# Optimization experiments

Hardware: AMD Instinct MI355X
Metric: run time of the kernel (lower is better)

## Reference

```python
import jax, jax.numpy as jnp
import numpy as np

NORMALIZED_LENGTH = 512  # init kwarg
T_FRAMES = 32768
N_LM = 543  # mediapipe holistic landmark count


def setup_inputs() -> dict:
    key = jax.random.key(0)
    kf, kn, kd, ki = jax.random.split(key, 4)
    frames = jax.random.uniform(kf, (T_FRAMES, N_LM, 3), dtype=jnp.float32)
    nan_mask = jax.random.uniform(kn, (T_FRAMES, N_LM, 3)) < 0.10
    frames = jnp.where(nan_mask, jnp.float32(jnp.nan), frames)
    drop = jax.random.uniform(kd, (T_FRAMES,)) < 0.05
    hand_zone = jnp.arange(N_LM) >= 468
    frames = jnp.where(drop[:, None, None] & hand_zone[None, :, None], jnp.float32(jnp.nan), frames)
    lips_idx = jax.random.randint(ki, (40,), 0, 468, dtype=jnp.int32)
    return {"frames": frames, "lips_idx": lips_idx}


def _nan_mean0(x):
    # tf_nan_mean over axis 0 (keepdims); 0/0 -> NaN in TF is immediately zeroed
    # afterwards, so we emit 0 directly (identical forward values, safe grads).
    finite = ~jnp.isnan(x)
    s = jnp.where(finite, x, jnp.zeros((), x.dtype)).sum(axis=0, keepdims=True)
    c = finite.sum(axis=0, keepdims=True)
    return jnp.where(c == 0, jnp.zeros((), x.dtype), s / jnp.maximum(c, 1).astype(x.dtype))


def reference(frames, lips_idx):
    fr = frames[:, :, :2]                       # drop z coord
    lh = fr[:, 468:489]                         # [T, 21, 2]
    rh = fr[:, 522:543]                         # [T, 21, 2]
    lh = jnp.stack([lh[..., 0], 1.0 - lh[..., 1]], axis=-1)
    rh = jnp.stack([1.0 - rh[..., 0], 1.0 - rh[..., 1]], axis=-1)
    # stack hands, NaN->0, sum over the 2-hand axis
    hand = jnp.nan_to_num(lh) + jnp.nan_to_num(rh)   # [T, 21, 2]
    keep = hand.sum(axis=(1, 2)) != 0.0              # frames with >=1 visible hand
    hand = hand[keep]                                # [S, 21, 2]
    lips = fr[:, lips_idx][keep]                     # [S, 40, 2]
    lips = jnp.where(jnp.isnan(lips), _nan_mean0(lips), lips)
    raw = jnp.concatenate([hand, lips], axis=1)      # [S, 61, 2]
    S = int(raw.shape[0])
    # tf.linspace(0, S-1, L+1) cast to int32 -> segment boundaries (truncation)
    b = np.linspace(0.0, S - 1.0, NORMALIZED_LENGTH + 1).astype(np.int32)
    # frame t belongs to bin i with b[i] <= t < b[i+1]; t >= b[L] maps to L (dropped)
    seg = jnp.asarray(np.searchsorted(b, np.arange(S), side="right") - 1)
    sums = jax.ops.segment_sum(raw, seg, num_segments=NORMALIZED_LENGTH)
    cnt = jax.ops.segment_sum(jnp.ones((S,), raw.dtype), seg, num_segments=NORMALIZED_LENGTH)
    # raw is NaN-free at this point, so nan-mean == plain mean; empty bin -> NaN -> 0
    mean = jnp.where(cnt[:, None, None] == 0, jnp.zeros((), raw.dtype),
                     sums / jnp.maximum(cnt, 1.0)[:, None, None])
    sampled = mean.reshape(NORMALIZED_LENGTH, -1)    # Flatten -> [L, 122]
    rows = sampled.sum(axis=1) != 0.0                # drop all-zero (empty) bins
    return sampled[rows]
```

## Files before the change

### kernel.cpp

```cpp
#include <hip/hip_runtime.h>

#define T_FRAMES 32768
#define ROWF 1629
#define FACEF 1404
#define NSEG 512
#define NVAL 122
#define STRIDE 128
#define K1_BLOCKS 512

__global__ __launch_bounds__(512) void k1_face(
    const float* __restrict__ frames, const int* __restrict__ lips_idx,
    int* __restrict__ keep, float* __restrict__ psum, int* __restrict__ pcnt,
    float* __restrict__ stage) {
  __shared__ float face[8][FACEF + 4];
  __shared__ float ls[80];
  __shared__ int lc[80];
  __shared__ int idx3[40];
  int tid = threadIdx.x;
  if (tid < 80) { ls[tid] = 0.0f; lc[tid] = 0; }
  if (tid < 40) idx3[tid] = lips_idx[tid] * 3;
  __syncthreads();

  int lane = tid & 63;
  int wv = tid >> 6;
  float* fb = face[wv];

  int jh = lane >> 1, ch = lane & 1;
  int offL = 1404 + 3 * jh + ch;
  int offR = 1566 + 3 * jh + ch;
  int offA = idx3[lane >> 1] + (lane & 1);
  int offB = (lane < 16) ? (idx3[(lane + 64) >> 1] + (lane & 1)) : 0;

  int base_t = (blockIdx.x * 8 + wv) * 8;
  for (int ff = 0; ff < 8; ++ff) {
    int t = base_t + ff;
    const float* f = frames + (size_t)t * ROWF;

    float lh = 0.0f, rh = 1.0f;
    if (lane < 42) { lh = f[offL]; rh = f[offR]; }

    for (int p = lane; p < FACEF; p += 64) fb[p] = f[p];

    float hv = 0.0f;
    if (lane < 42) {
      float a = ch ? (1.0f - lh) : lh;
      float b = 1.0f - rh;
      a = (a == a) ? a : 0.0f;
      b = (b == b) ? b : 0.0f;
      hv = a + b;
    }
    int kp = (__ballot(hv != 0.0f) != 0ull) ? 1 : 0;
    if (lane == 0) keep[t] = kp;

    if (kp) {
      float* srow = stage + (size_t)t * STRIDE;
      if (lane < 42) srow[lane] = hv;
      float x = fb[offA];
      srow[42 + lane] = x;
      if (x == x) { atomicAdd(&ls[lane], x); atomicAdd(&lc[lane], 1); }
      if (lane < 16) {
        float y = fb[offB];
        srow[106 + lane] = y;
        if (y == y) { atomicAdd(&ls[64 + lane], y); atomicAdd(&lc[64 + lane], 1); }
      }
    }
  }

  __syncthreads();
  if (tid < 80) {
    psum[blockIdx.x * 80 + tid] = ls[tid];
    pcnt[blockIdx.x * 80 + tid] = lc[tid];
  }
}

__global__ __launch_bounds__(1024) void k2_scan(
    const int* __restrict__ keep, int* __restrict__ kept_t,
    int* __restrict__ Sp, const float* __restrict__ psum,
    const int* __restrict__ pcnt, float* __restrict__ lip_sum,
    int* __restrict__ lip_cnt) {
  __shared__ int wsum[16];
  int tid = threadIdx.x;
  int lane = tid & 63, wv = tid >> 6;

  if (tid < 80) {
    float s = 0.0f; int c = 0;
    for (int b = 0; b < K1_BLOCKS; ++b) {
      s += psum[b * 80 + tid];
      c += pcnt[b * 80 + tid];
    }
    lip_sum[tid] = s; lip_cnt[tid] = c;
  }

  const int PER = T_FRAMES / 1024;
  int base = tid * PER;
  int fl[PER];
  int local = 0;
  #pragma unroll
  for (int k = 0; k < PER; ++k) { fl[k] = keep[base + k]; local += fl[k]; }

  int scan = local;
  #pragma unroll
  for (int off = 1; off < 64; off <<= 1) {
    int n = __shfl_up(scan, off);
    if (lane >= off) scan += n;
  }
  if (lane == 63) wsum[wv] = scan;
  __syncthreads();
  if (tid < 16) {
    int v = wsum[tid];
    #pragma unroll
    for (int off = 1; off < 16; off <<= 1) {
      int n = __shfl_up(v, off);
      if (tid >= off) v += n;
    }
    wsum[tid] = v;
  }
  __syncthreads();
  int excl = ((wv == 0) ? 0 : wsum[wv - 1]) + (scan - local);
  #pragma unroll
  for (int k = 0; k < PER; ++k) {
    if (fl[k]) kept_t[excl++] = base + k;
  }
  if (tid == 1023) Sp[0] = wsum[15];
}

__global__ __launch_bounds__(512) void k3_segments(
    const float* __restrict__ stage, const int* __restrict__ kept_t,
    const int* __restrict__ Sp, const float* __restrict__ lip_sum,
    const int* __restrict__ lip_cnt, float* __restrict__ out, int out_size) {
  __shared__ int seglist[128];
  __shared__ float part[4][128];
  int tid = threadIdx.x;
  int v = tid & 127;
  int r = tid >> 7;
  int seg = blockIdx.x;
  long long Sm1 = (long long)Sp[0] - 1;
  if (Sm1 < 0) Sm1 = 0;
  int lo = (int)(((long long)seg * Sm1) >> 9);
  int hi = (int)(((long long)(seg + 1) * Sm1) >> 9);
  int cnt = hi - lo;

  for (int k = tid; k < cnt; k += 512) seglist[k] = kept_t[lo + k];
  __syncthreads();

  float cm = 0.0f;
  if (v >= 42 && v < NVAL) {
    int w = v - 42;
    int c = lip_cnt[w];
    cm = (c == 0) ? 0.0f : lip_sum[w] / (float)c;
  }

  float acc = 0.0f;
  if (v < NVAL) {
    for (int k = r; k < cnt; k += 4) {
      float x = stage[(size_t)seglist[k] * STRIDE + v];
      acc += (x == x) ? x : cm;
    }
  }
  part[r][v] = acc;
  __syncthreads();
  if (r == 0 && v < NVAL) {
    float tot = part[0][v] + part[1][v] + part[2][v] + part[3][v];
    float mean = (cnt == 0) ? 0.0f : tot / (float)cnt;
    int o = seg * NVAL + v;
    if (o < out_size) out[o] = mean;
  }
}

extern "C" void kernel_launch(void* const* d_in, const int* in_sizes, int n_in,
                              void* d_out, int out_size, void* d_ws, size_t ws_size,
                              hipStream_t stream) {
  const float* frames = (const float*)d_in[0];
  const int* lips_idx = (const int*)d_in[1];
  float* out = (float*)d_out;

  char* ws = (char*)d_ws;
  int* keep      = (int*)(ws);
  int* kept_t    = (int*)(ws + 131072);
  int* Sp        = (int*)(ws + 262144);
  float* lip_sum = (float*)(ws + 262208);
  int* lip_cnt   = (int*)(ws + 262720);
  float* psum    = (float*)(ws + 263232);
  int* pcnt      = (int*)(ws + 427072);
  float* stage   = (float*)(ws + 590912);


  k1_face<<<K1_BLOCKS, 512, 0, stream>>>(frames, lips_idx, keep, psum,
                                         pcnt, stage);
  k2_scan<<<1, 1024, 0, stream>>>(keep, kept_t, Sp, psum, pcnt, lip_sum,
                                  lip_cnt);
  k3_segments<<<NSEG, 512, 0, stream>>>(stage, kept_t, Sp, lip_sum, lip_cnt,
                                        out, out_size);
}
```

Before: 344.0 us.

## Register-stage face rows with a column-to-slot map instead of shared-memory copy

The first kernel now gives each wavefront a single frame in a 1024-thread block with more blocks. It loads the 1404 face values into registers rather than copying them to LDS. A shared column-to-output-slot map, built once per block by one thread, scatters the lip values straight from registers. This removes the LDS round trip and increases memory-level parallelism, at the cost of more register pressure and a serial map build. The second kernel parallelises the reduction of the now four-times-larger per-block partial sums across 960 threads, and the workspace offsets move to fit them.

```diff
diff --git a/kernel.cpp b/kernel.cpp
--- a/kernel.cpp
+++ b/kernel.cpp
@@ -6,66 +6,97 @@
 #define NSEG 512
 #define NVAL 122
 #define STRIDE 128
-#define K1_BLOCKS 512
-
-__global__ __launch_bounds__(512) void k1_face(
+#define K1_BLOCKS 2048
+
+__global__ __launch_bounds__(1024) void k1_filter(
     const float* __restrict__ frames, const int* __restrict__ lips_idx,
     int* __restrict__ keep, float* __restrict__ psum, int* __restrict__ pcnt,
     float* __restrict__ stage) {
-  __shared__ float face[8][FACEF + 4];
+  __shared__ unsigned int cmap[FACEF];
   __shared__ float ls[80];
   __shared__ int lc[80];
   __shared__ int idx3[40];
   int tid = threadIdx.x;
   if (tid < 80) { ls[tid] = 0.0f; lc[tid] = 0; }
   if (tid < 40) idx3[tid] = lips_idx[tid] * 3;
+  for (int i = tid; i < FACEF; i += 1024) cmap[i] = 0xFFFFFFFFu;
+  __syncthreads();
+  if (tid == 0) {
+    for (int j = 0; j < 40; ++j) {
+      #pragma unroll
+      for (int c = 0; c < 2; ++c) {
+        int col = idx3[j] + c;
+        unsigned int v = 42u + 2u * j + c;
+        unsigned int w = cmap[col];
+        #pragma unroll
+        for (int b = 0; b < 4; ++b) {
+          if (((w >> (8 * b)) & 255u) == 255u) {
+            w = (w & ~(255u << (8 * b))) | (v << (8 * b));
+            break;
+          }
+        }
+        cmap[col] = w;
+      }
+    }
+  }
   __syncthreads();
 
   int lane = tid & 63;
   int wv = tid >> 6;
-  float* fb = face[wv];
+  int t = blockIdx.x * 16 + wv;
+  const float* f = frames + (size_t)t * ROWF;
 
   int jh = lane >> 1, ch = lane & 1;
   int offL = 1404 + 3 * jh + ch;
   int offR = 1566 + 3 * jh + ch;
-  int offA = idx3[lane >> 1] + (lane & 1);
-  int offB = (lane < 16) ? (idx3[(lane + 64) >> 1] + (lane & 1)) : 0;
-
-  int base_t = (blockIdx.x * 8 + wv) * 8;
-  for (int ff = 0; ff < 8; ++ff) {
-    int t = base_t + ff;
-    const float* f = frames + (size_t)t * ROWF;
-
-    float lh = 0.0f, rh = 1.0f;
-    if (lane < 42) { lh = f[offL]; rh = f[offR]; }
-
-    for (int p = lane; p < FACEF; p += 64) fb[p] = f[p];
-
-    float hv = 0.0f;
-    if (lane < 42) {
-      float a = ch ? (1.0f - lh) : lh;
-      float b = 1.0f - rh;
-      a = (a == a) ? a : 0.0f;
-      b = (b == b) ? b : 0.0f;
-      hv = a + b;
-    }
-    int kp = (__ballot(hv != 0.0f) != 0ull) ? 1 : 0;
-    if (lane == 0) keep[t] = kp;
-
-    if (kp) {
-      float* srow = stage + (size_t)t * STRIDE;
-      if (lane < 42) srow[lane] = hv;
-      float x = fb[offA];
-      srow[42 + lane] = x;
-      if (x == x) { atomicAdd(&ls[lane], x); atomicAdd(&lc[lane], 1); }
-      if (lane < 16) {
-        float y = fb[offB];
-        srow[106 + lane] = y;
-        if (y == y) { atomicAdd(&ls[64 + lane], y); atomicAdd(&lc[64 + lane], 1); }
+  float lh = 0.0f, rh = 1.0f;
+  if (lane < 42) { lh = f[offL]; rh = f[offR]; }
+
+  float xr[22];
+  #pragma unroll
+  for (int k = 0; k < 22; ++k) {
+    int p = lane + (k << 6);
+    if (p < FACEF) xr[k] = f[p];
+    else xr[k] = 0.0f;
+  }
+
+  float hv = 0.0f;
+  if (lane < 42) {
+    float a = ch ? (1.0f - lh) : lh;
+    float b = 1.0f - rh;
+    a = (a == a) ? a : 0.0f;
+    b = (b == b) ? b : 0.0f;
+    hv = a + b;
+  }
+  int kp = (__ballot(hv != 0.0f) != 0ull) ? 1 : 0;
+  if (lane == 0) keep[t] = kp;
+
+  if (kp) {
+    float* srow = stage + (size_t)t * STRIDE;
+    if (lane < 42) srow[lane] = hv;
+    #pragma unroll
+    for (int k = 0; k < 22; ++k) {
+      int p = lane + (k << 6);
+      if (p < FACEF) {
+        unsigned int m = cmap[p];
+        if (m != 0xFFFFFFFFu) {
+          float x = xr[k];
+          bool fin = (x == x);
+          #pragma unroll
+          for (int b = 0; b < 4; ++b) {
+            unsigned int s = (m >> (8 * b)) & 255u;
+            if (s != 255u) {
+              srow[s] = x;
+              if (fin) {
+                atomicAdd(&ls[s - 42], x);
+                atomicAdd(&lc[s - 42], 1);
+              }
+            }
+          }
+        }
       }
     }
   }
-
   __syncthreads();
   if (tid < 80) {
     psum[blockIdx.x * 80 + tid] = ls[tid];
@@ -78,16 +109,26 @@
     int* __restrict__ Sp, const float* __restrict__ psum,
     const int* __restrict__ pcnt, float* __restrict__ lip_sum,
     int* __restrict__ lip_cnt) {
+  __shared__ float psh[12][80];
+  __shared__ int csh[12][80];
   __shared__ int wsum[16];
   int tid = threadIdx.x;
   int lane = tid & 63, wv = tid >> 6;
 
+  if (tid < 960) {
+    int col = tid % 80, g = tid / 80;
+    float s = 0.0f; int c = 0;
+    for (int b = g; b < K1_BLOCKS; b += 12) {
+      s += psum[b * 80 + col];
+      c += pcnt[b * 80 + col];
+    }
+    psh[g][col] = s; csh[g][col] = c;
+  }
+  __syncthreads();
   if (tid < 80) {
     float s = 0.0f; int c = 0;
-    for (int b = 0; b < K1_BLOCKS; ++b) {
-      s += psum[b * 80 + tid];
-      c += pcnt[b * 80 + tid];
-    }
+    #pragma unroll
+    for (int g = 0; g < 12; ++g) { s += psh[g][tid]; c += csh[g][tid]; }
     lip_sum[tid] = s; lip_cnt[tid] = c;
   }
 
@@ -181,12 +222,12 @@
   float* lip_sum = (float*)(ws + 262208);
   int* lip_cnt   = (int*)(ws + 262720);
   float* psum    = (float*)(ws + 263232);
-  int* pcnt      = (int*)(ws + 427072);
-  float* stage   = (float*)(ws + 590912);
-
-
-  k1_face<<<K1_BLOCKS, 512, 0, stream>>>(frames, lips_idx, keep, psum,
-                                         pcnt, stage);
+  int* pcnt      = (int*)(ws + 918592);
+  float* stage   = (float*)(ws + 1573952);
+
+
+  k1_filter<<<K1_BLOCKS, 1024, 0, stream>>>(frames, lips_idx, keep, psum,
+                                            pcnt, stage);
   k2_scan<<<1, 1024, 0, stream>>>(keep, kept_t, Sp, psum, pcnt, lip_sum,
                                   lip_cnt);
   k3_segments<<<NSEG, 512, 0, stream>>>(stage, kept_t, Sp, lip_sum, lip_cnt,
```

Result: slower. 394.8 us (+14.8%).
